# Kernel tuning notes

Measured on AMD Instinct MI355X. Metric: run time of the kernel, lower is better.

## Reference

```python
import jax, jax.numpy as jnp
import numpy as np

LN_EPS = 1e-5

def setup_inputs() -> dict:
    key = jax.random.key(0)
    ks = jax.random.split(key, 8)
    B, N, C = 8, 16384, 256
    x = jax.random.normal(ks[0], (B, N, C), dtype=jnp.float32)
    time_decay = jax.random.normal(ks[1], (C,), dtype=jnp.float32) * 0.1
    s = 1.0 / np.sqrt(C)
    W_k = jax.random.normal(ks[2], (C, C), dtype=jnp.float32) * s
    W_v = jax.random.normal(ks[3], (C, C), dtype=jnp.float32) * s
    W_r = jax.random.normal(ks[4], (C, C), dtype=jnp.float32) * s
    W_o = jax.random.normal(ks[5], (C, C), dtype=jnp.float32) * s
    ln_w = jnp.ones((C,), dtype=jnp.float32)
    ln_b = jnp.zeros((C,), dtype=jnp.float32)
    return {"x": x, "time_decay": time_decay, "W_k": W_k, "W_v": W_v,
            "W_r": W_r, "W_o": W_o, "ln_w": ln_w, "ln_b": ln_b}

def _layernorm(x, w, b):
    mu = jnp.mean(x, axis=-1, keepdims=True)
    var = jnp.mean(jnp.square(x - mu), axis=-1, keepdims=True)
    return (x - mu) * jax.lax.rsqrt(var + LN_EPS) * w + b

def reference(x, time_decay, W_k, W_v, W_r, W_o, ln_w, ln_b):
    # x: (B, N, C)
    xn = _layernorm(x, ln_w, ln_b)
    k = jnp.einsum('bnc,dc->bnd', xn, W_k)
    v = jnp.einsum('bnc,dc->bnd', xn, W_v)
    r = jax.nn.sigmoid(jnp.einsum('bnc,dc->bnd', xn, W_r))
    decay = jnp.exp(-jax.nn.relu(time_decay))  # (C,)

    def step(state, k_t):
        state = state * decay + k_t  # (B, C)
        return state, state

    k_tm = jnp.swapaxes(k, 0, 1)  # (N, B, C) time-major for scan
    init = jnp.zeros(k.shape[::2], dtype=x.dtype)  # (B, C)
    _, states = jax.lax.scan(step, init, k_tm)
    states = jnp.swapaxes(states, 0, 1)  # (B, N, C)
    y = r * (states + v)
    y = jnp.einsum('bnc,dc->bnd', y, W_o)
    return y
```

## Files before the change

kernel.cpp:

```cpp
#include <hip/hip_runtime.h>
#include <hip/hip_bf16.h>
#include <stdint.h>


typedef __attribute__((ext_vector_type(8))) short short8;
typedef __attribute__((ext_vector_type(4))) short short4v;
typedef __attribute__((ext_vector_type(4))) float f32x4;

static __device__ __forceinline__ unsigned short f2bf(float f) {
  __hip_bfloat16 h = __float2bfloat16(f);
  return *reinterpret_cast<unsigned short*>(&h);
}
static __device__ __forceinline__ float bf2f(unsigned short u) {
  unsigned int v = ((unsigned int)u) << 16;
  float f;
  __builtin_memcpy(&f, &v, 4);
  return f;
}

__global__ void ln_kernel(const float* __restrict__ x,
                          const float* __restrict__ w,
                          const float* __restrict__ b,
                          unsigned short* __restrict__ xn) {
  const int wv = threadIdx.x >> 6;
  const int ln = threadIdx.x & 63;
  const size_t row = (size_t)blockIdx.x * 4 + wv;
  const float4 v = reinterpret_cast<const float4*>(x)[row * 64 + ln];
  float s  = v.x + v.y + v.z + v.w;
  float sq = v.x * v.x + v.y * v.y + v.z * v.z + v.w * v.w;
#pragma unroll
  for (int off = 32; off; off >>= 1) {
    s  += __shfl_xor(s, off, 64);
    sq += __shfl_xor(sq, off, 64);
  }
  const float mu  = s * (1.0f / 256.0f);
  const float var = sq * (1.0f / 256.0f) - mu * mu;
  const float rs  = rsqrtf(var + 1e-5f);
  const float4 w4 = reinterpret_cast<const float4*>(w)[ln];
  const float4 b4 = reinterpret_cast<const float4*>(b)[ln];
  ushort4 o;
  o.x = f2bf((v.x - mu) * rs * w4.x + b4.x);
  o.y = f2bf((v.y - mu) * rs * w4.y + b4.y);
  o.z = f2bf((v.z - mu) * rs * w4.z + b4.z);
  o.w = f2bf((v.w - mu) * rs * w4.w + b4.w);
  reinterpret_cast<ushort4*>(xn)[row * 64 + ln] = o;
}

__global__ void cvt_weights(const float* __restrict__ Wk,
                            const float* __restrict__ Wv,
                            const float* __restrict__ Wr,
                            const float* __restrict__ Wo,
                            unsigned short* __restrict__ Wkvr,
                            unsigned short* __restrict__ Wob) {
  const int idx = blockIdx.x * 256 + threadIdx.x;
  if (idx < 768 * 256) {
    const int r = idx >> 8;
    const int c = idx & 255;
    const float* src = (r < 256) ? Wk : ((r < 512) ? Wv : Wr);
    Wkvr[idx] = f2bf(src[(r & 255) * 256 + c]);
  } else {
    const int j = idx - 768 * 256;
    Wob[j] = f2bf(Wo[j]);
  }
}

template <int EPI, int NY>
__global__ __launch_bounds__(512, 4) void gemm_bt(
    const unsigned short* __restrict__ A,
    const unsigned short* __restrict__ Bt,
    unsigned short* __restrict__ kbuf,
    unsigned short* __restrict__ vbuf,
    unsigned short* __restrict__ rbuf,
    float* __restrict__ outf) {
  constexpr int K = 256;
  __shared__ unsigned short Als[128][256];

  const int tid = threadIdx.x;
  const int wv = tid >> 6;
  const int ln = tid & 63;
  const int cpx = (int)gridDim.x >> 3;
  const int hw = (int)blockIdx.x;
  const int bid = (hw & 7) * cpx + (hw >> 3);
  const int bm0 = (bid / NY) * 128;
  const int bn0 = (bid % NY) * 256;
  const int lq = ln >> 4;
  const int lm = ln & 15;

  f32x4 acc[4][4];
#pragma unroll
  for (int i = 0; i < 4; ++i)
#pragma unroll
    for (int j = 0; j < 4; ++j) acc[i][j] = (f32x4){0.f, 0.f, 0.f, 0.f};

  const int m0w = (wv >> 2) * 64;
  const int n0w = (wv & 3) * 64;

  {
    const int rsub = ln >> 5;
    const int p = ln & 31;
#pragma unroll
    for (int i = 0; i < 8; ++i) {
      const int r0 = wv * 16 + i * 2;
      const int r = r0 + rsub;
      const unsigned short* gA =
          A + (size_t)(bm0 + r) * K + ((p ^ (r & 7)) * 8);
      __builtin_amdgcn_global_load_lds(
          (const __attribute__((address_space(1))) void*)gA,
          (__attribute__((address_space(3))) void*)&Als[r0][0], 16, 0, 0);
    }
  }
  __syncthreads();

  const unsigned short* Bbase =
      Bt + (size_t)(bn0 + n0w + lm) * K + lq * 8;
#pragma unroll 2
  for (int ks = 0; ks < 8; ++ks) {
    short8 bfr[4], af[4];
#pragma unroll
    for (int t = 0; t < 4; ++t)
      bfr[t] = *reinterpret_cast<const short8*>(Bbase + (size_t)t * 16 * K +
                                                ks * 32);
#pragma unroll
    for (int t = 0; t < 4; ++t) {
      const int row = m0w + t * 16 + lm;
      af[t] = *reinterpret_cast<const short8*>(
          &Als[row][(((ks << 2) + lq) ^ (row & 7)) * 8]);
    }
#pragma unroll
    for (int mt = 0; mt < 4; ++mt)
#pragma unroll
      for (int nt = 0; nt < 4; ++nt)
        acc[mt][nt] = __builtin_amdgcn_mfma_f32_16x16x32_bf16(
            bfr[nt], af[mt], acc[mt][nt], 0, 0, 0);
  }

#pragma unroll
  for (int mt = 0; mt < 4; ++mt) {
    const int m_g = bm0 + m0w + mt * 16 + lm;
#pragma unroll
    for (int nt = 0; nt < 4; ++nt) {
      const int col = n0w + nt * 16 + lq * 4;
      f32x4 a = acc[mt][nt];
      if (EPI == 0) {
        const int bufi = bn0 >> 8;
        unsigned short* dst = (bufi == 0) ? kbuf : ((bufi == 1) ? vbuf : rbuf);
        if (bufi == 2) {
#pragma unroll
          for (int r = 0; r < 4; ++r) a[r] = 1.0f / (1.0f + __expf(-a[r]));
        }
        ushort4 pk;
        pk.x = f2bf(a[0]); pk.y = f2bf(a[1]); pk.z = f2bf(a[2]); pk.w = f2bf(a[3]);
        *reinterpret_cast<ushort4*>(&dst[(size_t)m_g * 256 + col]) = pk;
      } else {
        float4 o = make_float4(a[0], a[1], a[2], a[3]);
        *reinterpret_cast<float4*>(&outf[(size_t)m_g * 256 + col]) = o;
      }
    }
  }
}

__global__ void scan_carry(const unsigned short* __restrict__ k,
                           const float* __restrict__ td,
                           float* __restrict__ carry) {
  const int ln = threadIdx.x & 63;
  const int w = threadIdx.x >> 6;
  const int bch = blockIdx.x * 4 + w;
  const int c0 = ln * 4;
  float d[4], s[4];
#pragma unroll
  for (int j = 0; j < 4; ++j) {
    d[j] = expf(-fmaxf(td[c0 + j], 0.0f));
    s[j] = 0.0f;
  }
  const unsigned short* kp = k + (size_t)bch * 64 * 256 + c0;
#pragma unroll 8
  for (int i = 0; i < 64; ++i) {
    short4v kv = *reinterpret_cast<const short4v*>(kp + (size_t)i * 256);
#pragma unroll
    for (int j = 0; j < 4; ++j) s[j] = s[j] * d[j] + bf2f((unsigned short)kv[j]);
  }
  *reinterpret_cast<float4*>(carry + (size_t)bch * 256 + c0) =
      make_float4(s[0], s[1], s[2], s[3]);
}

__global__ void scan_chunks(float* __restrict__ carry,
                            const float* __restrict__ td) {
  const int b = blockIdx.x;
  const int c = threadIdx.x;
  const float dL = expf(-fmaxf(td[c], 0.0f) * 64.0f);
  float s = 0.0f;
  float* base = carry + (size_t)b * 256 * 256 + c;
  for (int j0 = 0; j0 < 256; j0 += 8) {
    float buf[8];
#pragma unroll
    for (int t = 0; t < 8; ++t) buf[t] = base[(size_t)(j0 + t) * 256];
#pragma unroll
    for (int t = 0; t < 8; ++t) {
      base[(size_t)(j0 + t) * 256] = s;
      s = dL * s + buf[t];
    }
  }
}

__global__ void scan_final(unsigned short* __restrict__ k,
                           const unsigned short* __restrict__ v,
                           const unsigned short* __restrict__ r,
                           const float* __restrict__ carryin,
                           const float* __restrict__ td) {
  const int ln = threadIdx.x & 63;
  const int w = threadIdx.x >> 6;
  const int bch = blockIdx.x * 4 + w;
  const int c0 = ln * 4;
  float d[4], s[4];
  const float4 ci = *reinterpret_cast<const float4*>(
      carryin + (size_t)bch * 256 + c0);
  s[0] = ci.x; s[1] = ci.y; s[2] = ci.z; s[3] = ci.w;
#pragma unroll
  for (int j = 0; j < 4; ++j) d[j] = expf(-fmaxf(td[c0 + j], 0.0f));
  const size_t base = (size_t)bch * 64 * 256 + c0;
#pragma unroll 4
  for (int i = 0; i < 64; ++i) {
    const size_t off = base + (size_t)i * 256;
    short4v kv = *reinterpret_cast<const short4v*>(k + off);
    short4v vv = *reinterpret_cast<const short4v*>(v + off);
    short4v rv = *reinterpret_cast<const short4v*>(r + off);
    short4v y;
#pragma unroll
    for (int j = 0; j < 4; ++j) {
      s[j] = s[j] * d[j] + bf2f((unsigned short)kv[j]);
      const float yj = bf2f((unsigned short)rv[j]) * (s[j] + bf2f((unsigned short)vv[j]));
      y[j] = (short)f2bf(yj);
    }
    *reinterpret_cast<short4v*>(k + off) = y;
  }
}

extern "C" void kernel_launch(void* const* d_in, const int* in_sizes, int n_in,
                              void* d_out, int out_size, void* d_ws, size_t ws_size,
                              hipStream_t stream) {
  const float* x   = (const float*)d_in[0];
  const float* td  = (const float*)d_in[1];
  const float* Wk  = (const float*)d_in[2];
  const float* Wv  = (const float*)d_in[3];
  const float* Wr  = (const float*)d_in[4];
  const float* Wo  = (const float*)d_in[5];
  const float* lnw = (const float*)d_in[6];
  const float* lnb = (const float*)d_in[7];
  float* out = (float*)d_out;

  const int Bsz = 8, C = 256;
  const size_t M = 131072;

  char* ws = (char*)d_ws;
  size_t off = 0;
  auto alloc = [&](size_t bytes) -> char* {
    char* p = ws + off;
    off += (bytes + 255) & ~(size_t)255;
    return p;
  };
  unsigned short* xn   = (unsigned short*)alloc(M * C * 2);
  unsigned short* kbuf = (unsigned short*)alloc(M * C * 2);
  unsigned short* vbuf = (unsigned short*)alloc(M * C * 2);
  unsigned short* rbuf = (unsigned short*)alloc(M * C * 2);
  unsigned short* Wkvr = (unsigned short*)alloc(768 * 256 * 2);
  unsigned short* Wob  = (unsigned short*)alloc(256 * 256 * 2);
  float* carry = (float*)alloc((size_t)Bsz * 256 * C * 4);
  (void)ws_size; (void)in_sizes; (void)n_in; (void)out_size;

  cvt_weights<<<dim3(1024), dim3(256), 0, stream>>>(Wk, Wv, Wr, Wo, Wkvr, Wob);
  ln_kernel<<<dim3((unsigned)(M / 4)), dim3(256), 0, stream>>>(x, lnw, lnb, xn);
  gemm_bt<0, 3><<<dim3(3072), dim3(512), 0, stream>>>(
      xn, Wkvr, kbuf, vbuf, rbuf, nullptr);
  scan_carry<<<dim3(512), dim3(256), 0, stream>>>(kbuf, td, carry);
  scan_chunks<<<dim3(Bsz), dim3(256), 0, stream>>>(carry, td);
  scan_final<<<dim3(512), dim3(256), 0, stream>>>(kbuf, vbuf, rbuf, carry, td);
  gemm_bt<1, 1><<<dim3(1024), dim3(512), 0, stream>>>(
      kbuf, Wob, nullptr, nullptr, nullptr, out);
}
```

Before: 493.2 us.

## Restructure GEMM to stage 256 full rows of A once and loop over N

The GEMM kernel now has each block load a 256-row slice of A (the full K=256) into LDS once, split into four 64-column panels. It then iterates over 64-column slices of the output, loading that slice's B fragments into registers for each pass. A is read from global memory only once, where previously it was reloaded for each of the 3 N-tiles, and the grid shrinks to 512 blocks with launch bounds relaxed to 2 waves per SIMD. In exchange, each block uses 128KB of LDS, occupancy drops, a 32-entry B fragment array puts pressure on registers, and B is re-fetched from global or cache on every pass.

```diff
diff --git a/kernel.cpp b/kernel.cpp
--- a/kernel.cpp
+++ b/kernel.cpp
@@ -64,96 +64,103 @@
   }
 }
 
-template <int EPI, int NY>
-__global__ __launch_bounds__(512, 4) void gemm_bt(
+template <int EPI, int NPASS>
+__global__ __launch_bounds__(512, 2) void gemm_bt(
     const unsigned short* __restrict__ A,
     const unsigned short* __restrict__ Bt,
     unsigned short* __restrict__ kbuf,
     unsigned short* __restrict__ vbuf,
     unsigned short* __restrict__ rbuf,
     float* __restrict__ outf) {
-  constexpr int K = 256;
-  __shared__ unsigned short Als[128][256];
+  __shared__ unsigned short Als[4][256][64];
 
   const int tid = threadIdx.x;
   const int wv = tid >> 6;
   const int ln = tid & 63;
-  const int cpx = (int)gridDim.x >> 3;
-  const int hw = (int)blockIdx.x;
-  const int bid = (hw & 7) * cpx + (hw >> 3);
-  const int bm0 = (bid / NY) * 128;
-  const int bn0 = (bid % NY) * 256;
   const int lq = ln >> 4;
   const int lm = ln & 15;
-
-  f32x4 acc[4][4];
-#pragma unroll
-  for (int i = 0; i < 4; ++i)
-#pragma unroll
-    for (int j = 0; j < 4; ++j) acc[i][j] = (f32x4){0.f, 0.f, 0.f, 0.f};
-
-  const int m0w = (wv >> 2) * 64;
-  const int n0w = (wv & 3) * 64;
+  const size_t mrow = (size_t)blockIdx.x * 256;
 
   {
-    const int rsub = ln >> 5;
-    const int p = ln & 31;
-#pragma unroll
-    for (int i = 0; i < 8; ++i) {
-      const int r0 = wv * 16 + i * 2;
-      const int r = r0 + rsub;
-      const unsigned short* gA =
-          A + (size_t)(bm0 + r) * K + ((p ^ (r & 7)) * 8);
-      __builtin_amdgcn_global_load_lds(
-          (const __attribute__((address_space(1))) void*)gA,
-          (__attribute__((address_space(3))) void*)&Als[r0][0], 16, 0, 0);
+    const int srow = ln >> 3;
+    const int schunk = (ln & 7) ^ srow;
+#pragma unroll
+    for (int p = 0; p < 4; ++p) {
+#pragma unroll
+      for (int i = 0; i < 4; ++i) {
+        const int r0 = wv * 32 + i * 8;
+        const unsigned short* gA =
+            A + (mrow + r0 + srow) * 256 + p * 64 + schunk * 8;
+        __builtin_amdgcn_global_load_lds(
+            (const __attribute__((address_space(1))) void*)gA,
+            (__attribute__((address_space(3))) void*)&Als[p][r0][0], 16, 0, 0);
+      }
     }
   }
   __syncthreads();
 
-  const unsigned short* Bbase =
-      Bt + (size_t)(bn0 + n0w + lm) * K + lq * 8;
-#pragma unroll 2
-  for (int ks = 0; ks < 8; ++ks) {
-    short8 bfr[4], af[4];
-#pragma unroll
-    for (int t = 0; t < 4; ++t)
-      bfr[t] = *reinterpret_cast<const short8*>(Bbase + (size_t)t * 16 * K +
-                                                ks * 32);
-#pragma unroll
-    for (int t = 0; t < 4; ++t) {
-      const int row = m0w + t * 16 + lm;
-      af[t] = *reinterpret_cast<const short8*>(
-          &Als[row][(((ks << 2) + lq) ^ (row & 7)) * 8]);
-    }
-#pragma unroll
-    for (int mt = 0; mt < 4; ++mt)
+  const int mw = wv * 32;
+
+  for (int ns = 0; ns < NPASS; ++ns) {
+    const int nb = ns * 64;
+
+    short8 Bf[8][4];
+#pragma unroll
+    for (int ks = 0; ks < 8; ++ks)
 #pragma unroll
       for (int nt = 0; nt < 4; ++nt)
-        acc[mt][nt] = __builtin_amdgcn_mfma_f32_16x16x32_bf16(
-            bfr[nt], af[mt], acc[mt][nt], 0, 0, 0);
-  }
-
-#pragma unroll
-  for (int mt = 0; mt < 4; ++mt) {
-    const int m_g = bm0 + m0w + mt * 16 + lm;
-#pragma unroll
-    for (int nt = 0; nt < 4; ++nt) {
-      const int col = n0w + nt * 16 + lq * 4;
-      f32x4 a = acc[mt][nt];
-      if (EPI == 0) {
-        const int bufi = bn0 >> 8;
-        unsigned short* dst = (bufi == 0) ? kbuf : ((bufi == 1) ? vbuf : rbuf);
-        if (bufi == 2) {
-#pragma unroll
-          for (int r = 0; r < 4; ++r) a[r] = 1.0f / (1.0f + __expf(-a[r]));
+        Bf[ks][nt] = *reinterpret_cast<const short8*>(
+            Bt + (size_t)(nb + nt * 16 + lm) * 256 + ks * 32 + lq * 8);
+
+    f32x4 acc[2][4];
+#pragma unroll
+    for (int t = 0; t < 2; ++t)
+#pragma unroll
+      for (int nt = 0; nt < 4; ++nt) acc[t][nt] = (f32x4){0.f, 0.f, 0.f, 0.f};
+
+#pragma unroll
+    for (int p = 0; p < 4; ++p) {
+#pragma unroll
+      for (int h = 0; h < 2; ++h) {
+        const int ks = p * 2 + h;
+        short8 af[2];
+#pragma unroll
+        for (int t = 0; t < 2; ++t) {
+          const int row = mw + t * 16 + lm;
+          const int chunk = (h * 4 + lq) ^ (row & 7);
+          af[t] = *reinterpret_cast<const short8*>(&Als[p][row][chunk * 8]);
         }
-        ushort4 pk;
-        pk.x = f2bf(a[0]); pk.y = f2bf(a[1]); pk.z = f2bf(a[2]); pk.w = f2bf(a[3]);
-        *reinterpret_cast<ushort4*>(&dst[(size_t)m_g * 256 + col]) = pk;
-      } else {
-        float4 o = make_float4(a[0], a[1], a[2], a[3]);
-        *reinterpret_cast<float4*>(&outf[(size_t)m_g * 256 + col]) = o;
+#pragma unroll
+        for (int t = 0; t < 2; ++t)
+#pragma unroll
+          for (int nt = 0; nt < 4; ++nt)
+            acc[t][nt] = __builtin_amdgcn_mfma_f32_16x16x32_bf16(
+                Bf[ks][nt], af[t], acc[t][nt], 0, 0, 0);
+      }
+    }
+
+#pragma unroll
+    for (int t = 0; t < 2; ++t) {
+      const size_t m_g = mrow + mw + t * 16 + lm;
+#pragma unroll
+      for (int nt = 0; nt < 4; ++nt) {
+        f32x4 a = acc[t][nt];
+        if (EPI == 0) {
+          const int bufi = nb >> 8;
+          const int col = (nb & 255) + nt * 16 + lq * 4;
+          unsigned short* dst = (bufi == 0) ? kbuf : ((bufi == 1) ? vbuf : rbuf);
+          if (bufi == 2) {
+#pragma unroll
+            for (int r = 0; r < 4; ++r) a[r] = 1.0f / (1.0f + __expf(-a[r]));
+          }
+          ushort4 pk;
+          pk.x = f2bf(a[0]); pk.y = f2bf(a[1]); pk.z = f2bf(a[2]); pk.w = f2bf(a[3]);
+          *reinterpret_cast<ushort4*>(&dst[m_g * 256 + col]) = pk;
+        } else {
+          const int col = nb + nt * 16 + lq * 4;
+          float4 o = make_float4(a[0], a[1], a[2], a[3]);
+          *reinterpret_cast<float4*>(&outf[m_g * 256 + col]) = o;
+        }
       }
     }
   }
@@ -269,11 +276,11 @@
 
   cvt_weights<<<dim3(1024), dim3(256), 0, stream>>>(Wk, Wv, Wr, Wo, Wkvr, Wob);
   ln_kernel<<<dim3((unsigned)(M / 4)), dim3(256), 0, stream>>>(x, lnw, lnb, xn);
-  gemm_bt<0, 3><<<dim3(3072), dim3(512), 0, stream>>>(
+  gemm_bt<0, 12><<<dim3(512), dim3(512), 0, stream>>>(
       xn, Wkvr, kbuf, vbuf, rbuf, nullptr);
   scan_carry<<<dim3(512), dim3(256), 0, stream>>>(kbuf, td, carry);
   scan_chunks<<<dim3(Bsz), dim3(256), 0, stream>>>(carry, td);
   scan_final<<<dim3(512), dim3(256), 0, stream>>>(kbuf, vbuf, rbuf, carry, td);
-  gemm_bt<1, 1><<<dim3(1024), dim3(512), 0, stream>>>(
+  gemm_bt<1, 4><<<dim3(512), dim3(512), 0, stream>>>(
       kbuf, Wob, nullptr, nullptr, nullptr, out);
 }
```

After: 588.1 us. 1.19x slower.
